# Optimization experiments

Hardware: AMD Instinct MI355X
Metric: run time of the kernel (lower is better)

## Reference

```python
import jax, jax.numpy as jnp
import numpy as np

N_NODES = 100_000
N_EDGES = 1_600_000
F_IN = 32
F_OUT = 32


def setup_inputs() -> dict:
    key = jax.random.key(0)
    kx, kr, kc, kv, kw = jax.random.split(key, 5)
    x = jax.random.normal(kx, (N_NODES, F_IN), dtype=jnp.float32)
    # COO adjacency: rows sorted (CSR-like locality), cols random, positive norm weights
    rows = jnp.sort(jax.random.randint(kr, (N_EDGES,), 0, N_NODES, dtype=jnp.int64))
    cols = jax.random.randint(kc, (N_EDGES,), 0, N_NODES, dtype=jnp.int64)
    vals = jax.random.uniform(kv, (N_EDGES,), dtype=jnp.float32)
    weight = jax.random.normal(kw, (F_IN, F_OUT), dtype=jnp.float32) / np.sqrt(F_IN)
    return {"x": x, "rows": rows, "cols": cols, "vals": vals, "weight": weight}


def reference(x, rows, cols, vals, weight):
    # z = A_hat @ x  (COO SpMM, equivalent to the distributed gather+spmm+allreduce)
    gathered = x[cols] * vals[:, None]                       # [E, F_in] edge messages
    z = jax.ops.segment_sum(gathered, rows, num_segments=x.shape[0])  # [N, F_in]
    # feature transform: z @ W (done in GCNFunc after broad_func)
    return z @ weight                                        # [N, F_out]
```

## Files before the change

kernel.cpp:

```cpp
#include <hip/hip_runtime.h>

#define F 32

typedef float v2f __attribute__((ext_vector_type(2)));

__device__ __forceinline__ unsigned int f2bf_rne(float f) {
    unsigned int u = __float_as_uint(f);
    return (u + 0x7fffu + ((u >> 16) & 1u)) >> 16;
}
__device__ __forceinline__ float bf_lo(unsigned int u) { return __uint_as_float(u << 16); }
__device__ __forceinline__ float bf_hi(unsigned int u) { return __uint_as_float(u & 0xffff0000u); }

__global__ void prep_kernel(const float* __restrict__ x, const float* __restrict__ w,
                            uint4* __restrict__ y4,
                            const int* __restrict__ rows,
                            int* __restrict__ row_ptr,
                            int n_nodes, int n_edges, int gxw) {
    int b = blockIdx.x;
    if (b < gxw) {
        int n = b * blockDim.x + threadIdx.x;
        if (n >= n_nodes) return;
        const float4* xp = (const float4*)(x + (size_t)n * F);
        float xr[F];
#pragma unroll
        for (int j = 0; j < 8; ++j) {
            float4 t = xp[j];
            xr[4*j+0] = t.x; xr[4*j+1] = t.y; xr[4*j+2] = t.z; xr[4*j+3] = t.w;
        }
        float acc[F];
#pragma unroll
        for (int f = 0; f < F; ++f) acc[f] = 0.f;
#pragma unroll
        for (int k = 0; k < F; ++k) {
            float xk = xr[k];
#pragma unroll
            for (int f = 0; f < F; ++f)
                acc[f] = fmaf(xk, w[k * F + f], acc[f]);
        }
        unsigned int op[16];
#pragma unroll
        for (int k = 0; k < 16; ++k)
            op[k] = f2bf_rne(acc[2*k]) | (f2bf_rne(acc[2*k+1]) << 16);
#pragma unroll
        for (int j = 0; j < 4; ++j)
            y4[(size_t)n * 4 + j] = make_uint4(op[4*j], op[4*j+1], op[4*j+2], op[4*j+3]);
    } else {
        int e = (b - gxw) * blockDim.x + threadIdx.x;
        if (e > n_edges) return;
        int prev = (e == 0) ? -1 : rows[e - 1];
        int cur  = (e == n_edges) ? n_nodes : rows[e];
        for (int r = prev + 1; r <= cur; ++r) row_ptr[r] = e;
    }
}

__global__ void spmm_kernel(const unsigned int* __restrict__ y_u,
                            const int* __restrict__ cols,
                            const float* __restrict__ vals,
                            const int* __restrict__ row_ptr,
                            v2f* __restrict__ out2, int n_nodes) {
    int gid = blockIdx.x * blockDim.x + threadIdx.x;
    int n = gid >> 4;
    int l = gid & 15;
    if (n >= n_nodes) return;

    int e0 = row_ptr[n];
    int e1 = row_ptr[n + 1];
    float aL = 0.f, aH = 0.f;

    for (int base = e0; base < e1; base += 16) {
        int idx  = base + l;
        bool ok  = idx < e1;
        int idxc = ok ? idx : (e1 - 1);
        int   cB = __builtin_nontemporal_load(&cols[idxc]);
        float vB = ok ? __builtin_nontemporal_load(&vals[idxc]) : 0.f;

        unsigned int u[16];
#pragma unroll
        for (int j = 0; j < 16; ++j) {
            int c = __shfl(cB, j, 16);
            u[j] = y_u[(size_t)c * 16 + l];
        }
#pragma unroll
        for (int j = 0; j < 16; ++j) {
            float v = __shfl(vB, j, 16);
            aL += bf_lo(u[j]) * v;
            aH += bf_hi(u[j]) * v;
        }
    }
    v2f o; o[0] = aL; o[1] = aH;
    __builtin_nontemporal_store(o, &out2[(size_t)n * 16 + l]);
}

extern "C" void kernel_launch(void* const* d_in, const int* in_sizes, int n_in,
                              void* d_out, int out_size, void* d_ws, size_t ws_size,
                              hipStream_t stream) {
    const float* x    = (const float*)d_in[0];
    const int*   rows = (const int*)d_in[1];
    const int*   cols = (const int*)d_in[2];
    const float* vals = (const float*)d_in[3];
    const float* w    = (const float*)d_in[4];

    int n_nodes = in_sizes[0] / F;
    int n_edges = in_sizes[1];

    uint4* y4      = (uint4*)d_ws;
    int*   row_ptr = (int*)((char*)d_ws + (size_t)n_nodes * 16 * sizeof(unsigned int));

    int gxw = (n_nodes + 255) / 256;
    int gpe = (n_edges + 1 + 255) / 256;
    prep_kernel<<<gxw + gpe, 256, 0, stream>>>(x, w, y4, rows, row_ptr,
                                               n_nodes, n_edges, gxw);

    int grid_spmm = (n_nodes * 16 + 255) / 256;
    spmm_kernel<<<grid_spmm, 256, 0, stream>>>((const unsigned int*)y4, cols, vals,
                                               row_ptr, (v2f*)d_out, n_nodes);
}
```

Baseline: 51.16 us.

## Switch SpMM from row-parallel CSR to edge-parallel with segmented atomics

The SpMM now assigns fixed 16-edge chunks to each 16-lane group instead of one node per group. Within a chunk it accumulates a partial sum while the row index stays the same, and flushes to the output with float atomicAdd whenever the row changes. This drops the row_ptr construction pass and balances work across rows whose degrees vary. In exchange the prep kernel must zero the output, and the SpMM pays for extra atomic traffic with a non-deterministic summation order.

```diff
diff --git a/kernel.cpp b/kernel.cpp
--- a/kernel.cpp
+++ b/kernel.cpp
@@ -1,8 +1,6 @@
 #include <hip/hip_runtime.h>
 
 #define F 32
-
-typedef float v2f __attribute__((ext_vector_type(2)));
 
 __device__ __forceinline__ unsigned int f2bf_rne(float f) {
     unsigned int u = __float_as_uint(f);
@@ -13,9 +11,8 @@
 
 __global__ void prep_kernel(const float* __restrict__ x, const float* __restrict__ w,
                             uint4* __restrict__ y4,
-                            const int* __restrict__ rows,
-                            int* __restrict__ row_ptr,
-                            int n_nodes, int n_edges, int gxw) {
+                            uint4* __restrict__ out_z,
+                            int n_nodes, int n_out4, int gxw) {
     int b = blockIdx.x;
     if (b < gxw) {
         int n = b * blockDim.x + threadIdx.x;
@@ -45,50 +42,52 @@
         for (int j = 0; j < 4; ++j)
             y4[(size_t)n * 4 + j] = make_uint4(op[4*j], op[4*j+1], op[4*j+2], op[4*j+3]);
     } else {
-        int e = (b - gxw) * blockDim.x + threadIdx.x;
-        if (e > n_edges) return;
-        int prev = (e == 0) ? -1 : rows[e - 1];
-        int cur  = (e == n_edges) ? n_nodes : rows[e];
-        for (int r = prev + 1; r <= cur; ++r) row_ptr[r] = e;
+        int i = (b - gxw) * blockDim.x + threadIdx.x;
+        if (i < n_out4) out_z[i] = make_uint4(0u, 0u, 0u, 0u);
     }
 }
 
 __global__ void spmm_kernel(const unsigned int* __restrict__ y_u,
                             const int* __restrict__ cols,
                             const float* __restrict__ vals,
-                            const int* __restrict__ row_ptr,
-                            v2f* __restrict__ out2, int n_nodes) {
-    int gid = blockIdx.x * blockDim.x + threadIdx.x;
-    int n = gid >> 4;
-    int l = gid & 15;
-    if (n >= n_nodes) return;
+                            const int* __restrict__ rows,
+                            float* __restrict__ out, int n_edges) {
+    int gid   = blockIdx.x * blockDim.x + threadIdx.x;
+    int tid   = threadIdx.x & 63;
+    int l     = tid & 15;
+    int gbase = tid & 48;
+    long base = (long)(gid >> 6) * 64;
 
-    int e0 = row_ptr[n];
-    int e1 = row_ptr[n + 1];
-    float aL = 0.f, aH = 0.f;
+    int eidx = (int)base + tid;
+    bool ok  = eidx < n_edges;
+    int ecl  = ok ? eidx : (n_edges - 1);
+    int   cB = cols[ecl];
+    int   rB = rows[ecl];
+    float vB = ok ? vals[ecl] : 0.f;
 
-    for (int base = e0; base < e1; base += 16) {
-        int idx  = base + l;
-        bool ok  = idx < e1;
-        int idxc = ok ? idx : (e1 - 1);
-        int   cB = __builtin_nontemporal_load(&cols[idxc]);
-        float vB = ok ? __builtin_nontemporal_load(&vals[idxc]) : 0.f;
+    unsigned int u[16];
+#pragma unroll
+    for (int j = 0; j < 16; ++j) {
+        int c = __shfl(cB, gbase + j, 64);
+        u[j] = y_u[(size_t)c * 16 + l];
+    }
 
-        unsigned int u[16];
+    float a0 = 0.f, a1 = 0.f;
+    int rprev = __shfl(rB, gbase, 64);
 #pragma unroll
-        for (int j = 0; j < 16; ++j) {
-            int c = __shfl(cB, j, 16);
-            u[j] = y_u[(size_t)c * 16 + l];
+    for (int j = 0; j < 16; ++j) {
+        int   r = __shfl(rB, gbase + j, 64);
+        float v = __shfl(vB, gbase + j, 64);
+        if (r != rprev) {
+            atomicAdd(&out[(size_t)rprev * F + 2 * l],     a0);
+            atomicAdd(&out[(size_t)rprev * F + 2 * l + 1], a1);
+            a0 = 0.f; a1 = 0.f; rprev = r;
         }
-#pragma unroll
-        for (int j = 0; j < 16; ++j) {
-            float v = __shfl(vB, j, 16);
-            aL += bf_lo(u[j]) * v;
-            aH += bf_hi(u[j]) * v;
-        }
+        a0 += bf_lo(u[j]) * v;
+        a1 += bf_hi(u[j]) * v;
     }
-    v2f o; o[0] = aL; o[1] = aH;
-    __builtin_nontemporal_store(o, &out2[(size_t)n * 16 + l]);
+    atomicAdd(&out[(size_t)rprev * F + 2 * l],     a0);
+    atomicAdd(&out[(size_t)rprev * F + 2 * l + 1], a1);
 }
 
 extern "C" void kernel_launch(void* const* d_in, const int* in_sizes, int n_in,
@@ -103,15 +102,16 @@
     int n_nodes = in_sizes[0] / F;
     int n_edges = in_sizes[1];
 
-    uint4* y4      = (uint4*)d_ws;
-    int*   row_ptr = (int*)((char*)d_ws + (size_t)n_nodes * 16 * sizeof(unsigned int));
+    uint4* y4 = (uint4*)d_ws;
 
+    int n_out4 = out_size / 4;
     int gxw = (n_nodes + 255) / 256;
-    int gpe = (n_edges + 1 + 255) / 256;
-    prep_kernel<<<gxw + gpe, 256, 0, stream>>>(x, w, y4, rows, row_ptr,
-                                               n_nodes, n_edges, gxw);
+    int gz  = (n_out4 + 255) / 256;
+    prep_kernel<<<gxw + gz, 256, 0, stream>>>(x, w, y4, (uint4*)d_out,
+                                              n_nodes, n_out4, gxw);
 
-    int grid_spmm = (n_nodes * 16 + 255) / 256;
+    long waves = ((long)n_edges + 63) / 64;
+    int grid_spmm = (int)((waves * 64 + 255) / 256);
     spmm_kernel<<<grid_spmm, 256, 0, stream>>>((const unsigned int*)y4, cols, vals,
-                                               row_ptr, (v2f*)d_out, n_nodes);
+                                               rows, (float*)d_out, n_edges);
 }
```

Result: slower. 74.94 us (+46.5%).
